# Performance work log

Measured on AMD Instinct MI355X. Metric: run time of the kernel, lower is better.

## Reference

```python
import jax, jax.numpy as jnp
import numpy as np

N = 100000
E = 1600000
F_IN = 32
F_OUT = 32


def setup_inputs() -> dict:
    key = jax.random.key(0)
    ks = jax.random.split(key, 12)
    x = jax.random.normal(ks[0], (N, F_IN), jnp.float32)
    edge_index = jax.random.randint(ks[1], (2, E), 0, N)
    edge_weight = jax.random.uniform(ks[2], (E,), jnp.float32)
    s = 0.1
    return {
        "x": x,
        "edge_index": edge_index,
        "edge_weight": edge_weight,
        "Wz": jax.random.normal(ks[3], (F_IN, F_OUT), jnp.float32) * s,
        "bz": jnp.zeros((F_OUT,), jnp.float32),
        "Wr": jax.random.normal(ks[4], (F_IN, F_OUT), jnp.float32) * s,
        "br": jnp.zeros((F_OUT,), jnp.float32),
        "Wh": jax.random.normal(ks[5], (F_IN, F_OUT), jnp.float32) * s,
        "bh": jnp.zeros((F_OUT,), jnp.float32),
        "Lz_W": jax.random.normal(ks[6], (2 * F_OUT, F_OUT), jnp.float32) * s,
        "Lz_b": jnp.zeros((F_OUT,), jnp.float32),
        "Lr_W": jax.random.normal(ks[7], (2 * F_OUT, F_OUT), jnp.float32) * s,
        "Lr_b": jnp.zeros((F_OUT,), jnp.float32),
        "Lh_W": jax.random.normal(ks[8], (2 * F_OUT, F_OUT), jnp.float32) * s,
        "Lh_b": jnp.zeros((F_OUT,), jnp.float32),
        "lin_W": jax.random.normal(ks[9], (F_OUT, 1), jnp.float32) * s,
        "lin_b": jnp.zeros((1,), jnp.float32),
    }


def reference(x, edge_index, edge_weight, Wz, bz, Wr, br, Wh, bh,
              Lz_W, Lz_b, Lr_W, Lr_b, Lh_W, Lh_b, lin_W, lin_b):
    n = x.shape[0]
    f_out = Wz.shape[1]
    row, col = edge_index[0], edge_index[1]
    # GCN normalization with added self-loops (PyG gcn_norm, improved=False)
    loop = jnp.arange(n, dtype=row.dtype)
    row_ = jnp.concatenate([row, loop])
    col_ = jnp.concatenate([col, loop])
    ew = jnp.concatenate([edge_weight, jnp.ones((n,), edge_weight.dtype)])
    deg = jax.ops.segment_sum(ew, col_, num_segments=n)
    dinv = jnp.where(deg > 0, jax.lax.rsqrt(deg), 0.0)
    norm = dinv[row_] * ew * dinv[col_]  # [E+N]

    def conv(W, b):
        xw = x @ W                                   # [N, f_out]
        msg = xw[row_] * norm[:, None]               # gather + scale [E+N, f_out]
        return jax.ops.segment_sum(msg, col_, num_segments=n) + b

    H = jnp.zeros((n, f_out), x.dtype)  # TGCN default hidden state
    Z = jax.nn.sigmoid(jnp.concatenate([conv(Wz, bz), H], axis=1) @ Lz_W + Lz_b)
    R = jax.nn.sigmoid(jnp.concatenate([conv(Wr, br), H], axis=1) @ Lr_W + Lr_b)
    H_tilde = jnp.tanh(jnp.concatenate([conv(Wh, bh), H * R], axis=1) @ Lh_W + Lh_b)
    H = Z * H + (1.0 - Z) * H_tilde
    h = jax.nn.relu(H)
    return h @ lin_W + lin_b
```

## Files before the change

### kernel.cpp

```cpp
#include <hip/hip_runtime.h>
#include <hip/hip_fp16.h>
#include <math.h>

#define F 32
#define FC 64
#define MAXDEG 64
#define BINSHIFT 9
#define BINW 512
#define CHUNKS 256
#define CAP 12288

__device__ inline float h15_to_f(unsigned v) {
  __half_raw hr; hr.x = (unsigned short)(v & 0x7FFFu);
  return __half2float(*reinterpret_cast<__half*>(&hr));
}

__global__ void k_part(const int* __restrict__ ei, const float* __restrict__ ew,
                       int* __restrict__ binCnt, uint2* __restrict__ part,
                       int e_total, int chsz, int nb,
                       const float* __restrict__ Wz, const float* __restrict__ Wh,
                       const float* __restrict__ LzW, const float* __restrict__ LhW,
                       const float* __restrict__ bz, const float* __restrict__ bh,
                       const float* __restrict__ Lzb, const float* __restrict__ Lhb,
                       float* __restrict__ Mcomb, float* __restrict__ czh) {
  if ((int)blockIdx.x < CHUNKS) {
    __shared__ int hist[256];
    __shared__ int cursor[256];
    int t = threadIdx.x;
    hist[t] = 0;
    __syncthreads();
    int k = blockIdx.x;
    int lo = k * chsz;
    int hi = lo + chsz; if (hi > e_total) hi = e_total;
    for (int e = lo + t; e < hi; e += 256)
      atomicAdd(&hist[ei[e_total + e] >> BINSHIFT], 1);
    __syncthreads();
    if (t < nb) {
      int h = hist[t];
      cursor[t] = (h > 0) ? (t * CAP + atomicAdd(&binCnt[t], h)) : 0;
    }
    __syncthreads();
    for (int e = lo + t; e < hi; e += 256) {
      int r = ei[e];
      int c = ei[e_total + e];
      float w = ew[e];
      int b = c >> BINSHIFT;
      int pos = atomicAdd(&cursor[b], 1);
      uint2 v;
      v.x = ((unsigned)(c & (BINW - 1)) << 17) | (unsigned)r;
      v.y = __float_as_uint(w);
      part[pos] = v;
    }
    return;
  }
  int t = threadIdx.x;
  for (int idx = t; idx < F * FC; idx += blockDim.x) {
    int k = idx / FC, j = idx % FC;
    float s = 0.f;
    if (j < F) { for (int m = 0; m < F; ++m) s = fmaf(Wz[k*F+m], LzW[m*F+j], s); }
    else { int jj = j-F; for (int m = 0; m < F; ++m) s = fmaf(Wh[k*F+m], LhW[m*F+jj], s); }
    Mcomb[idx] = s;
  }
  if (t < FC) {
    float s;
    if (t < F) { s = Lzb[t]; for (int k = 0; k < F; ++k) s = fmaf(bz[k], LzW[k*F+t], s); }
    else { int jj = t-F; s = Lhb[jj]; for (int k = 0; k < F; ++k) s = fmaf(bh[k], LhW[k*F+jj], s); }
    czh[t] = s;
  }
}

__global__ void k_p4(const uint2* __restrict__ part, const int* __restrict__ binCnt,
                     unsigned* __restrict__ pk, unsigned long long* __restrict__ deg64,
                     int n) {
  __shared__ unsigned long long dg[BINW];
  int b = blockIdx.x, t = threadIdx.x;
  if (t < BINW) dg[t] = 0ull;
  __syncthreads();
  int lo = b * CAP, hi = lo + binCnt[b];
  for (int e = lo + t; e < hi; e += 1024) {
    uint2 v = part[e];
    unsigned r  = v.x & 0x1FFFFu;
    unsigned cl = v.x >> 17;
    float w = __uint_as_float(v.y);
    unsigned long long fx = (unsigned long long)((double)w * 4294967296.0) + (1ull << 48);
    unsigned long long old = atomicAdd(&dg[cl], fx);
    unsigned rank = (unsigned)(old >> 48);
    if (rank < MAXDEG) {
      unsigned hv = (unsigned)__half_as_ushort(__float2half(w)) & 0x7FFFu;
      unsigned c = ((unsigned)b << BINSHIFT) | cl;
      pk[((size_t)c << 6) | rank] = (r << 15) | hv;
    }
  }
  __syncthreads();
  int base = b << BINSHIFT;
  if (t < BINW) {
    int i = base + t;
    if (i < n) deg64[i] = dg[t];
  }
}

__global__ void k_xw(const float* __restrict__ x, const float* __restrict__ Mcomb,
                     const unsigned long long* __restrict__ deg64,
                     __half* __restrict__ XWs, int n) {
  __shared__ float M[F * FC];
  __shared__ float xt[32][F];
  int t = threadIdx.x;
  for (int u = t; u < F * FC; u += 256) M[u] = Mcomb[u];
  int tile = blockIdx.x << 5;
  {
    int node = t >> 3;
    if (tile + node < n)
      ((float4*)xt)[t] = ((const float4*)(x + (size_t)tile * F))[t];
  }
  __syncthreads();
  int j = t & 63;
  int g = t >> 6;
  float mcol[F];
#pragma unroll
  for (int k = 0; k < F; ++k) mcol[k] = M[k * FC + j];
#pragma unroll
  for (int u = 0; u < 8; ++u) {
    int node = (g << 3) + u;
    int i = tile + node;
    if (i >= n) break;
    float acc = 0.f;
#pragma unroll
    for (int k = 0; k < F; ++k) acc = fmaf(xt[node][k], mcol[k], acc);
    unsigned long long dv = deg64[i];
    float s = 1.0f + (float)((double)(dv & 0xFFFFFFFFFFFFull) * (1.0 / 4294967296.0));
    float di = rsqrtf(s);
    XWs[((size_t)i << 6) | j] = __float2half(di * acc);
  }
}

__global__ void __launch_bounds__(256, 8)
k_agg(const __half* __restrict__ XWs,
      const unsigned long long* __restrict__ deg64,
      const unsigned* __restrict__ pk,
      const float* __restrict__ czh,
      const float* __restrict__ linW, const float* __restrict__ linb,
      float* __restrict__ out, int n) {
  int wid = (blockIdx.x * blockDim.x + threadIdx.x) >> 6;
  int j = threadIdx.x & 63;
  if (wid >= n) return;
  unsigned long long dv = deg64[wid];
  int cnt = (int)(dv >> 48);
  cnt = (cnt > MAXDEG) ? MAXDEG : cnt;
  float s = 1.0f + (float)((double)(dv & 0xFFFFFFFFFFFFull) * (1.0 / 4294967296.0));
  float di = rsqrtf(s);
  unsigned pv = (j < cnt) ? pk[((size_t)wid << 6) | j] : 0u;
  const __half* lanebase = XWs + j;
  float acc0 = __half2float(lanebase[(size_t)wid << 6]);
  float acc1 = 0.f, acc2 = 0.f, acc3 = 0.f;
  int e = 0;
  for (; e + 16 <= cnt; e += 16) {
    unsigned v0  = __shfl(pv, e, 64);
    unsigned v1  = __shfl(pv, e + 1, 64);
    unsigned v2  = __shfl(pv, e + 2, 64);
    unsigned v3  = __shfl(pv, e + 3, 64);
    unsigned v4  = __shfl(pv, e + 4, 64);
    unsigned v5  = __shfl(pv, e + 5, 64);
    unsigned v6  = __shfl(pv, e + 6, 64);
    unsigned v7  = __shfl(pv, e + 7, 64);
    unsigned v8  = __shfl(pv, e + 8, 64);
    unsigned v9  = __shfl(pv, e + 9, 64);
    unsigned v10 = __shfl(pv, e + 10, 64);
    unsigned v11 = __shfl(pv, e + 11, 64);
    unsigned v12 = __shfl(pv, e + 12, 64);
    unsigned v13 = __shfl(pv, e + 13, 64);
    unsigned v14 = __shfl(pv, e + 14, 64);
    unsigned v15 = __shfl(pv, e + 15, 64);
    float f0  = __half2float(lanebase[(size_t)(v0  >> 15) << 6]);
    float f1  = __half2float(lanebase[(size_t)(v1  >> 15) << 6]);
    float f2  = __half2float(lanebase[(size_t)(v2  >> 15) << 6]);
    float f3  = __half2float(lanebase[(size_t)(v3  >> 15) << 6]);
    float f4  = __half2float(lanebase[(size_t)(v4  >> 15) << 6]);
    float f5  = __half2float(lanebase[(size_t)(v5  >> 15) << 6]);
    float f6  = __half2float(lanebase[(size_t)(v6  >> 15) << 6]);
    float f7  = __half2float(lanebase[(size_t)(v7  >> 15) << 6]);
    float f8  = __half2float(lanebase[(size_t)(v8  >> 15) << 6]);
    float f9  = __half2float(lanebase[(size_t)(v9  >> 15) << 6]);
    float f10 = __half2float(lanebase[(size_t)(v10 >> 15) << 6]);
    float f11 = __half2float(lanebase[(size_t)(v11 >> 15) << 6]);
    float f12 = __half2float(lanebase[(size_t)(v12 >> 15) << 6]);
    float f13 = __half2float(lanebase[(size_t)(v13 >> 15) << 6]);
    float f14 = __half2float(lanebase[(size_t)(v14 >> 15) << 6]);
    float f15 = __half2float(lanebase[(size_t)(v15 >> 15) << 6]);
    acc0 = fmaf(h15_to_f(v0),  f0,  acc0);
    acc1 = fmaf(h15_to_f(v1),  f1,  acc1);
    acc2 = fmaf(h15_to_f(v2),  f2,  acc2);
    acc3 = fmaf(h15_to_f(v3),  f3,  acc3);
    acc0 = fmaf(h15_to_f(v4),  f4,  acc0);
    acc1 = fmaf(h15_to_f(v5),  f5,  acc1);
    acc2 = fmaf(h15_to_f(v6),  f6,  acc2);
    acc3 = fmaf(h15_to_f(v7),  f7,  acc3);
    acc0 = fmaf(h15_to_f(v8),  f8,  acc0);
    acc1 = fmaf(h15_to_f(v9),  f9,  acc1);
    acc2 = fmaf(h15_to_f(v10), f10, acc2);
    acc3 = fmaf(h15_to_f(v11), f11, acc3);
    acc0 = fmaf(h15_to_f(v12), f12, acc0);
    acc1 = fmaf(h15_to_f(v13), f13, acc1);
    acc2 = fmaf(h15_to_f(v14), f14, acc2);
    acc3 = fmaf(h15_to_f(v15), f15, acc3);
  }
  for (; e + 8 <= cnt; e += 8) {
    unsigned v0 = __shfl(pv, e, 64);
    unsigned v1 = __shfl(pv, e + 1, 64);
    unsigned v2 = __shfl(pv, e + 2, 64);
    unsigned v3 = __shfl(pv, e + 3, 64);
    unsigned v4 = __shfl(pv, e + 4, 64);
    unsigned v5 = __shfl(pv, e + 5, 64);
    unsigned v6 = __shfl(pv, e + 6, 64);
    unsigned v7 = __shfl(pv, e + 7, 64);
    float f0 = __half2float(lanebase[(size_t)(v0 >> 15) << 6]);
    float f1 = __half2float(lanebase[(size_t)(v1 >> 15) << 6]);
    float f2 = __half2float(lanebase[(size_t)(v2 >> 15) << 6]);
    float f3 = __half2float(lanebase[(size_t)(v3 >> 15) << 6]);
    float f4 = __half2float(lanebase[(size_t)(v4 >> 15) << 6]);
    float f5 = __half2float(lanebase[(size_t)(v5 >> 15) << 6]);
    float f6 = __half2float(lanebase[(size_t)(v6 >> 15) << 6]);
    float f7 = __half2float(lanebase[(size_t)(v7 >> 15) << 6]);
    acc0 = fmaf(h15_to_f(v0), f0, acc0);
    acc1 = fmaf(h15_to_f(v1), f1, acc1);
    acc2 = fmaf(h15_to_f(v2), f2, acc2);
    acc3 = fmaf(h15_to_f(v3), f3, acc3);
    acc0 = fmaf(h15_to_f(v4), f4, acc0);
    acc1 = fmaf(h15_to_f(v5), f5, acc1);
    acc2 = fmaf(h15_to_f(v6), f6, acc2);
    acc3 = fmaf(h15_to_f(v7), f7, acc3);
  }
  for (; e + 4 <= cnt; e += 4) {
    unsigned v0 = __shfl(pv, e, 64);
    unsigned v1 = __shfl(pv, e + 1, 64);
    unsigned v2 = __shfl(pv, e + 2, 64);
    unsigned v3 = __shfl(pv, e + 3, 64);
    float f0 = __half2float(lanebase[(size_t)(v0 >> 15) << 6]);
    float f1 = __half2float(lanebase[(size_t)(v1 >> 15) << 6]);
    float f2 = __half2float(lanebase[(size_t)(v2 >> 15) << 6]);
    float f3 = __half2float(lanebase[(size_t)(v3 >> 15) << 6]);
    acc0 = fmaf(h15_to_f(v0), f0, acc0);
    acc1 = fmaf(h15_to_f(v1), f1, acc1);
    acc2 = fmaf(h15_to_f(v2), f2, acc2);
    acc3 = fmaf(h15_to_f(v3), f3, acc3);
  }
  for (; e < cnt; ++e) {
    unsigned v = __shfl(pv, e, 64);
    acc0 = fmaf(h15_to_f(v), __half2float(lanebase[(size_t)(v >> 15) << 6]), acc0);
  }
  float acc = ((acc0 + acc1) + (acc2 + acc3)) * di;
  float a = acc + czh[j];
  float g;
  if (j < 32) g = 1.0f / (1.0f + expf(-a));
  else        g = tanhf(a);
  float other = __shfl(g, (j + 32) & 63, 64);
  float val = 0.f;
  if (j < 32) {
    float hn = (1.0f - g) * other;
    val = fmaxf(hn, 0.f) * linW[j];
  }
#pragma unroll
  for (int d = 32; d > 0; d >>= 1) val += __shfl_xor(val, d, 64);
  if (j == 0) out[wid] = val + linb[0];
}

extern "C" void kernel_launch(void* const* d_in, const int* in_sizes, int n_in,
                              void* d_out, int out_size, void* d_ws, size_t ws_size,
                              hipStream_t stream) {
  const float* x   = (const float*)d_in[0];
  const int*   ei  = (const int*)d_in[1];
  const float* ew  = (const float*)d_in[2];
  const float* Wz  = (const float*)d_in[3];
  const float* bz  = (const float*)d_in[4];
  const float* Wh  = (const float*)d_in[7];
  const float* bh  = (const float*)d_in[8];
  const float* LzW = (const float*)d_in[9];
  const float* Lzb = (const float*)d_in[10];
  const float* LhW = (const float*)d_in[13];
  const float* Lhb = (const float*)d_in[14];
  const float* lnW = (const float*)d_in[15];
  const float* lnb = (const float*)d_in[16];
  float* out = (float*)d_out;

  const int n = in_sizes[0] / F;
  const int e_total = in_sizes[2];
  const int nb = (n + BINW - 1) >> BINSHIFT;
  const int chsz = (e_total + CHUNKS - 1) / CHUNKS;

  char* p = (char*)d_ws;
  auto alloc = [&](size_t bytes) -> void* {
    void* q = (void*)p;
    p += (bytes + 255) & ~(size_t)255;
    return q;
  };
  float* Mcomb  = (float*)alloc((size_t)F * FC * 4);
  float* czh    = (float*)alloc(FC * 4);
  unsigned long long* deg64 = (unsigned long long*)alloc((size_t)n * 8);
  int* binCnt   = (int*)alloc((size_t)nb * 4);
  uint2* part   = (uint2*)alloc((size_t)nb * CAP * 8);
  unsigned* pk  = (unsigned*)alloc(((size_t)n << 6) * 4);
  __half* XWs   = (__half*)part;

  dim3 blk(256);
  int nxblocks = (n + 31) >> 5;
  int wblocks = (int)(((size_t)n * 64 + 255) / 256);

  hipMemsetAsync(binCnt, 0, (size_t)nb * 4, stream);
  k_part<<<CHUNKS + 1, blk, 0, stream>>>(ei, ew, binCnt, part, e_total, chsz, nb,
      Wz, Wh, LzW, LhW, bz, bh, Lzb, Lhb, Mcomb, czh);
  k_p4<<<nb, 1024, 0, stream>>>(part, binCnt, pk, deg64, n);
  k_xw<<<nxblocks, blk, 0, stream>>>(x, Mcomb, deg64, XWs, n);
  k_agg<<<wblocks, blk, 0, stream>>>(XWs, deg64, pk, czh, lnW, lnb, out, n);
}
```

Measured before the change: 109.9 us.

## Split Z/H feature tables and aggregate two nodes per wavefront

The combined 64-wide half-precision XW table is split into separate 32-wide Z and H tables. Each wavefront now processes two destination nodes, one per 32-lane half, gathering first Z then H features for its node's neighbours. This makes each neighbour gather touch a single 64-byte row and doubles node-level parallelism per wave. The cost is two sequential gather passes with more loop iterations and extra handling for degrees above 32. The partition chunk count is also doubled.

```diff
diff --git a/kernel.cpp b/kernel.cpp
--- a/kernel.cpp
+++ b/kernel.cpp
@@ -7,7 +7,7 @@
 #define MAXDEG 64
 #define BINSHIFT 9
 #define BINW 512
-#define CHUNKS 256
+#define CHUNKS 512
 #define CAP 12288
 
 __device__ inline float h15_to_f(unsigned v) {
@@ -101,7 +101,7 @@
 
 __global__ void k_xw(const float* __restrict__ x, const float* __restrict__ Mcomb,
                      const unsigned long long* __restrict__ deg64,
-                     __half* __restrict__ XWs, int n) {
+                     __half* __restrict__ XWz, __half* __restrict__ XWh, int n) {
   __shared__ float M[F * FC];
   __shared__ float xt[32][F];
   int t = threadIdx.x;
@@ -118,6 +118,8 @@
   float mcol[F];
 #pragma unroll
   for (int k = 0; k < F; ++k) mcol[k] = M[k * FC + j];
+  __half* dst = (j < 32) ? XWz : XWh;
+  int f = j & 31;
 #pragma unroll
   for (int u = 0; u < 8; ++u) {
     int node = (g << 3) + u;
@@ -129,138 +131,126 @@
     unsigned long long dv = deg64[i];
     float s = 1.0f + (float)((double)(dv & 0xFFFFFFFFFFFFull) * (1.0 / 4294967296.0));
     float di = rsqrtf(s);
-    XWs[((size_t)i << 6) | j] = __float2half(di * acc);
+    dst[((size_t)i << 5) | f] = __float2half(di * acc);
   }
 }
 
 __global__ void __launch_bounds__(256, 8)
-k_agg(const __half* __restrict__ XWs,
+k_agg(const __half* __restrict__ XWz, const __half* __restrict__ XWh,
       const unsigned long long* __restrict__ deg64,
       const unsigned* __restrict__ pk,
       const float* __restrict__ czh,
       const float* __restrict__ linW, const float* __restrict__ linb,
       float* __restrict__ out, int n) {
-  int wid = (blockIdx.x * blockDim.x + threadIdx.x) >> 6;
+  int w = (blockIdx.x * blockDim.x + threadIdx.x) >> 6;
   int j = threadIdx.x & 63;
-  if (wid >= n) return;
-  unsigned long long dv = deg64[wid];
+  int hsel = j & 32;
+  int f = j & 31;
+  int wid = 2 * w + (hsel >> 5);
+  bool active = wid < n;
+  int widc = active ? wid : (n - 1);
+  unsigned long long dv = deg64[widc];
   int cnt = (int)(dv >> 48);
   cnt = (cnt > MAXDEG) ? MAXDEG : cnt;
   float s = 1.0f + (float)((double)(dv & 0xFFFFFFFFFFFFull) * (1.0 / 4294967296.0));
   float di = rsqrtf(s);
-  unsigned pv = (j < cnt) ? pk[((size_t)wid << 6) | j] : 0u;
-  const __half* lanebase = XWs + j;
-  float acc0 = __half2float(lanebase[(size_t)wid << 6]);
-  float acc1 = 0.f, acc2 = 0.f, acc3 = 0.f;
+  unsigned pv = (f < cnt) ? pk[((size_t)widc << 6) | f] : 0u;
+  int cA = __shfl(cnt, 0, 64), cB = __shfl(cnt, 32, 64);
+  int maxc = (cA > cB) ? cA : cB;
+  int m32 = (maxc < 32) ? maxc : 32;
+  unsigned pv2 = 0u;
+  if (maxc > 32) {
+    if (f < cnt - 32) pv2 = pk[((size_t)widc << 6) | (32 + f)];
+  }
+  const __half* zbase = XWz + f;
+  float az0 = __half2float(zbase[(size_t)widc << 5]);
+  float az1 = 0.f, az2 = 0.f, az3 = 0.f;
   int e = 0;
-  for (; e + 16 <= cnt; e += 16) {
-    unsigned v0  = __shfl(pv, e, 64);
-    unsigned v1  = __shfl(pv, e + 1, 64);
-    unsigned v2  = __shfl(pv, e + 2, 64);
-    unsigned v3  = __shfl(pv, e + 3, 64);
-    unsigned v4  = __shfl(pv, e + 4, 64);
-    unsigned v5  = __shfl(pv, e + 5, 64);
-    unsigned v6  = __shfl(pv, e + 6, 64);
-    unsigned v7  = __shfl(pv, e + 7, 64);
-    unsigned v8  = __shfl(pv, e + 8, 64);
-    unsigned v9  = __shfl(pv, e + 9, 64);
-    unsigned v10 = __shfl(pv, e + 10, 64);
-    unsigned v11 = __shfl(pv, e + 11, 64);
-    unsigned v12 = __shfl(pv, e + 12, 64);
-    unsigned v13 = __shfl(pv, e + 13, 64);
-    unsigned v14 = __shfl(pv, e + 14, 64);
-    unsigned v15 = __shfl(pv, e + 15, 64);
-    float f0  = __half2float(lanebase[(size_t)(v0  >> 15) << 6]);
-    float f1  = __half2float(lanebase[(size_t)(v1  >> 15) << 6]);
-    float f2  = __half2float(lanebase[(size_t)(v2  >> 15) << 6]);
-    float f3  = __half2float(lanebase[(size_t)(v3  >> 15) << 6]);
-    float f4  = __half2float(lanebase[(size_t)(v4  >> 15) << 6]);
-    float f5  = __half2float(lanebase[(size_t)(v5  >> 15) << 6]);
-    float f6  = __half2float(lanebase[(size_t)(v6  >> 15) << 6]);
-    float f7  = __half2float(lanebase[(size_t)(v7  >> 15) << 6]);
-    float f8  = __half2float(lanebase[(size_t)(v8  >> 15) << 6]);
-    float f9  = __half2float(lanebase[(size_t)(v9  >> 15) << 6]);
-    float f10 = __half2float(lanebase[(size_t)(v10 >> 15) << 6]);
-    float f11 = __half2float(lanebase[(size_t)(v11 >> 15) << 6]);
-    float f12 = __half2float(lanebase[(size_t)(v12 >> 15) << 6]);
-    float f13 = __half2float(lanebase[(size_t)(v13 >> 15) << 6]);
-    float f14 = __half2float(lanebase[(size_t)(v14 >> 15) << 6]);
-    float f15 = __half2float(lanebase[(size_t)(v15 >> 15) << 6]);
-    acc0 = fmaf(h15_to_f(v0),  f0,  acc0);
-    acc1 = fmaf(h15_to_f(v1),  f1,  acc1);
-    acc2 = fmaf(h15_to_f(v2),  f2,  acc2);
-    acc3 = fmaf(h15_to_f(v3),  f3,  acc3);
-    acc0 = fmaf(h15_to_f(v4),  f4,  acc0);
-    acc1 = fmaf(h15_to_f(v5),  f5,  acc1);
-    acc2 = fmaf(h15_to_f(v6),  f6,  acc2);
-    acc3 = fmaf(h15_to_f(v7),  f7,  acc3);
-    acc0 = fmaf(h15_to_f(v8),  f8,  acc0);
-    acc1 = fmaf(h15_to_f(v9),  f9,  acc1);
-    acc2 = fmaf(h15_to_f(v10), f10, acc2);
-    acc3 = fmaf(h15_to_f(v11), f11, acc3);
-    acc0 = fmaf(h15_to_f(v12), f12, acc0);
-    acc1 = fmaf(h15_to_f(v13), f13, acc1);
-    acc2 = fmaf(h15_to_f(v14), f14, acc2);
-    acc3 = fmaf(h15_to_f(v15), f15, acc3);
-  }
-  for (; e + 8 <= cnt; e += 8) {
-    unsigned v0 = __shfl(pv, e, 64);
-    unsigned v1 = __shfl(pv, e + 1, 64);
-    unsigned v2 = __shfl(pv, e + 2, 64);
-    unsigned v3 = __shfl(pv, e + 3, 64);
-    unsigned v4 = __shfl(pv, e + 4, 64);
-    unsigned v5 = __shfl(pv, e + 5, 64);
-    unsigned v6 = __shfl(pv, e + 6, 64);
-    unsigned v7 = __shfl(pv, e + 7, 64);
-    float f0 = __half2float(lanebase[(size_t)(v0 >> 15) << 6]);
-    float f1 = __half2float(lanebase[(size_t)(v1 >> 15) << 6]);
-    float f2 = __half2float(lanebase[(size_t)(v2 >> 15) << 6]);
-    float f3 = __half2float(lanebase[(size_t)(v3 >> 15) << 6]);
-    float f4 = __half2float(lanebase[(size_t)(v4 >> 15) << 6]);
-    float f5 = __half2float(lanebase[(size_t)(v5 >> 15) << 6]);
-    float f6 = __half2float(lanebase[(size_t)(v6 >> 15) << 6]);
-    float f7 = __half2float(lanebase[(size_t)(v7 >> 15) << 6]);
-    acc0 = fmaf(h15_to_f(v0), f0, acc0);
-    acc1 = fmaf(h15_to_f(v1), f1, acc1);
-    acc2 = fmaf(h15_to_f(v2), f2, acc2);
-    acc3 = fmaf(h15_to_f(v3), f3, acc3);
-    acc0 = fmaf(h15_to_f(v4), f4, acc0);
-    acc1 = fmaf(h15_to_f(v5), f5, acc1);
-    acc2 = fmaf(h15_to_f(v6), f6, acc2);
-    acc3 = fmaf(h15_to_f(v7), f7, acc3);
-  }
-  for (; e + 4 <= cnt; e += 4) {
-    unsigned v0 = __shfl(pv, e, 64);
-    unsigned v1 = __shfl(pv, e + 1, 64);
-    unsigned v2 = __shfl(pv, e + 2, 64);
-    unsigned v3 = __shfl(pv, e + 3, 64);
-    float f0 = __half2float(lanebase[(size_t)(v0 >> 15) << 6]);
-    float f1 = __half2float(lanebase[(size_t)(v1 >> 15) << 6]);
-    float f2 = __half2float(lanebase[(size_t)(v2 >> 15) << 6]);
-    float f3 = __half2float(lanebase[(size_t)(v3 >> 15) << 6]);
-    acc0 = fmaf(h15_to_f(v0), f0, acc0);
-    acc1 = fmaf(h15_to_f(v1), f1, acc1);
-    acc2 = fmaf(h15_to_f(v2), f2, acc2);
-    acc3 = fmaf(h15_to_f(v3), f3, acc3);
-  }
-  for (; e < cnt; ++e) {
-    unsigned v = __shfl(pv, e, 64);
-    acc0 = fmaf(h15_to_f(v), __half2float(lanebase[(size_t)(v >> 15) << 6]), acc0);
-  }
-  float acc = ((acc0 + acc1) + (acc2 + acc3)) * di;
-  float a = acc + czh[j];
-  float g;
-  if (j < 32) g = 1.0f / (1.0f + expf(-a));
-  else        g = tanhf(a);
-  float other = __shfl(g, (j + 32) & 63, 64);
-  float val = 0.f;
-  if (j < 32) {
-    float hn = (1.0f - g) * other;
-    val = fmaxf(hn, 0.f) * linW[j];
-  }
+  for (; e + 8 <= m32; e += 8) {
+    unsigned v0 = __shfl(pv, (e    ) | hsel, 64);
+    unsigned v1 = __shfl(pv, (e + 1) | hsel, 64);
+    unsigned v2 = __shfl(pv, (e + 2) | hsel, 64);
+    unsigned v3 = __shfl(pv, (e + 3) | hsel, 64);
+    unsigned v4 = __shfl(pv, (e + 4) | hsel, 64);
+    unsigned v5 = __shfl(pv, (e + 5) | hsel, 64);
+    unsigned v6 = __shfl(pv, (e + 6) | hsel, 64);
+    unsigned v7 = __shfl(pv, (e + 7) | hsel, 64);
+    float f0 = __half2float(zbase[(size_t)(v0 >> 15) << 5]);
+    float f1 = __half2float(zbase[(size_t)(v1 >> 15) << 5]);
+    float f2 = __half2float(zbase[(size_t)(v2 >> 15) << 5]);
+    float f3 = __half2float(zbase[(size_t)(v3 >> 15) << 5]);
+    float f4 = __half2float(zbase[(size_t)(v4 >> 15) << 5]);
+    float f5 = __half2float(zbase[(size_t)(v5 >> 15) << 5]);
+    float f6 = __half2float(zbase[(size_t)(v6 >> 15) << 5]);
+    float f7 = __half2float(zbase[(size_t)(v7 >> 15) << 5]);
+    az0 = fmaf(h15_to_f(v0), f0, az0);
+    az1 = fmaf(h15_to_f(v1), f1, az1);
+    az2 = fmaf(h15_to_f(v2), f2, az2);
+    az3 = fmaf(h15_to_f(v3), f3, az3);
+    az0 = fmaf(h15_to_f(v4), f4, az0);
+    az1 = fmaf(h15_to_f(v5), f5, az1);
+    az2 = fmaf(h15_to_f(v6), f6, az2);
+    az3 = fmaf(h15_to_f(v7), f7, az3);
+  }
+  for (; e < m32; ++e) {
+    unsigned v = __shfl(pv, e | hsel, 64);
+    az0 = fmaf(h15_to_f(v), __half2float(zbase[(size_t)(v >> 15) << 5]), az0);
+  }
+  if (maxc > 32) {
+    for (int e2 = 32; e2 < maxc; ++e2) {
+      unsigned v = __shfl(pv2, (e2 - 32) | hsel, 64);
+      az0 = fmaf(h15_to_f(v), __half2float(zbase[(size_t)(v >> 15) << 5]), az0);
+    }
+  }
+  float az = ((az0 + az1) + (az2 + az3)) * di;
+  const __half* hbase = XWh + f;
+  float ah0 = __half2float(hbase[(size_t)widc << 5]);
+  float ah1 = 0.f, ah2 = 0.f, ah3 = 0.f;
+  e = 0;
+  for (; e + 8 <= m32; e += 8) {
+    unsigned v0 = __shfl(pv, (e    ) | hsel, 64);
+    unsigned v1 = __shfl(pv, (e + 1) | hsel, 64);
+    unsigned v2 = __shfl(pv, (e + 2) | hsel, 64);
+    unsigned v3 = __shfl(pv, (e + 3) | hsel, 64);
+    unsigned v4 = __shfl(pv, (e + 4) | hsel, 64);
+    unsigned v5 = __shfl(pv, (e + 5) | hsel, 64);
+    unsigned v6 = __shfl(pv, (e + 6) | hsel, 64);
+    unsigned v7 = __shfl(pv, (e + 7) | hsel, 64);
+    float f0 = __half2float(hbase[(size_t)(v0 >> 15) << 5]);
+    float f1 = __half2float(hbase[(size_t)(v1 >> 15) << 5]);
+    float f2 = __half2float(hbase[(size_t)(v2 >> 15) << 5]);
+    float f3 = __half2float(hbase[(size_t)(v3 >> 15) << 5]);
+    float f4 = __half2float(hbase[(size_t)(v4 >> 15) << 5]);
+    float f5 = __half2float(hbase[(size_t)(v5 >> 15) << 5]);
+    float f6 = __half2float(hbase[(size_t)(v6 >> 15) << 5]);
+    float f7 = __half2float(hbase[(size_t)(v7 >> 15) << 5]);
+    ah0 = fmaf(h15_to_f(v0), f0, ah0);
+    ah1 = fmaf(h15_to_f(v1), f1, ah1);
+    ah2 = fmaf(h15_to_f(v2), f2, ah2);
+    ah3 = fmaf(h15_to_f(v3), f3, ah3);
+    ah0 = fmaf(h15_to_f(v4), f4, ah0);
+    ah1 = fmaf(h15_to_f(v5), f5, ah1);
+    ah2 = fmaf(h15_to_f(v6), f6, ah2);
+    ah3 = fmaf(h15_to_f(v7), f7, ah3);
+  }
+  for (; e < m32; ++e) {
+    unsigned v = __shfl(pv, e | hsel, 64);
+    ah0 = fmaf(h15_to_f(v), __half2float(hbase[(size_t)(v >> 15) << 5]), ah0);
+  }
+  if (maxc > 32) {
+    for (int e2 = 32; e2 < maxc; ++e2) {
+      unsigned v = __shfl(pv2, (e2 - 32) | hsel, 64);
+      ah0 = fmaf(h15_to_f(v), __half2float(hbase[(size_t)(v >> 15) << 5]), ah0);
+    }
+  }
+  float ah = ((ah0 + ah1) + (ah2 + ah3)) * di;
+  float gZ = 1.0f / (1.0f + expf(-(az + czh[f])));
+  float gH = tanhf(ah + czh[32 + f]);
+  float hn = (1.0f - gZ) * gH;
+  float val = active ? fmaxf(hn, 0.f) * linW[f] : 0.f;
 #pragma unroll
-  for (int d = 32; d > 0; d >>= 1) val += __shfl_xor(val, d, 64);
-  if (j == 0) out[wid] = val + linb[0];
+  for (int d = 16; d > 0; d >>= 1) val += __shfl_xor(val, d, 64);
+  if (f == 0 && active) out[wid] = val + linb[0];
 }
 
 extern "C" void kernel_launch(void* const* d_in, const int* in_sizes, int n_in,
@@ -298,16 +288,18 @@
   int* binCnt   = (int*)alloc((size_t)nb * 4);
   uint2* part   = (uint2*)alloc((size_t)nb * CAP * 8);
   unsigned* pk  = (unsigned*)alloc(((size_t)n << 6) * 4);
-  __half* XWs   = (__half*)part;
+  __half* XWz   = (__half*)part;
+  __half* XWh   = XWz + ((size_t)n << 5);
 
   dim3 blk(256);
   int nxblocks = (n + 31) >> 5;
-  int wblocks = (int)(((size_t)n * 64 + 255) / 256);
+  int apairs = (n + 1) >> 1;
+  int ablocks = (int)(((size_t)apairs * 64 + 255) / 256);
 
   hipMemsetAsync(binCnt, 0, (size_t)nb * 4, stream);
   k_part<<<CHUNKS + 1, blk, 0, stream>>>(ei, ew, binCnt, part, e_total, chsz, nb,
       Wz, Wh, LzW, LhW, bz, bh, Lzb, Lhb, Mcomb, czh);
   k_p4<<<nb, 1024, 0, stream>>>(part, binCnt, pk, deg64, n);
-  k_xw<<<nxblocks, blk, 0, stream>>>(x, Mcomb, deg64, XWs, n);
-  k_agg<<<wblocks, blk, 0, stream>>>(XWs, deg64, pk, czh, lnW, lnb, out, n);
-}
+  k_xw<<<nxblocks, blk, 0, stream>>>(x, Mcomb, deg64, XWz, XWh, n);
+  k_agg<<<ablocks, blk, 0, stream>>>(XWz, XWh, deg64, pk, czh, lnW, lnb, out, n);
+}
```

Result: slower. 119.5 us (+8.7%).
